# Optimization experiments

Hardware: AMD Instinct MI355X
Metric: run time of the kernel (lower is better)

The kernel has to match this reference:

```python
import jax, jax.numpy as jnp
import numpy as np

D = 768
NH = 8
HD = D // NH
DFF = 2048
EPS = 1e-5


def _layer_norm(x, g, b):
    mu = jnp.mean(x, axis=-1, keepdims=True)
    var = jnp.mean(jnp.square(x - mu), axis=-1, keepdims=True)
    return (x - mu) * jax.lax.rsqrt(var + EPS) * g + b


def setup_inputs() -> dict:
    key = jax.random.key(0)
    ks = jax.random.split(key, 16)
    B, L = 2, 2048
    s = 0.02
    return {
        "x": jax.random.normal(ks[0], (B, L, D), jnp.float32),
        "attn_bias": jax.random.normal(ks[1], (B, L, L), jnp.float32),
        "in_proj_w": jax.random.normal(ks[2], (3 * D, D), jnp.float32) * s,
        "in_proj_b": jnp.zeros((3 * D,), jnp.float32),
        "out_w": jax.random.normal(ks[3], (D, D), jnp.float32) * s,
        "out_b": jnp.zeros((D,), jnp.float32),
        "W1": jax.random.normal(ks[4], (DFF, D), jnp.float32) * s,
        "b1": jnp.zeros((DFF,), jnp.float32),
        "W2": jax.random.normal(ks[5], (D, DFF), jnp.float32) * s,
        "b2": jnp.zeros((D,), jnp.float32),
        "g1": jnp.ones((D,), jnp.float32),
        "be1": jnp.zeros((D,), jnp.float32),
        "g2": jnp.ones((D,), jnp.float32),
        "be2": jnp.zeros((D,), jnp.float32),
    }


def reference(x, attn_bias, in_proj_w, in_proj_b, out_w, out_b,
              W1, b1, W2, b2, g1, be1, g2, be2):
    B, L, _ = x.shape
    # fused qkv projection (torch nn.MultiheadAttention in_proj)
    qkv = x @ in_proj_w.T + in_proj_b          # [B, L, 3D]
    q, k, v = jnp.split(qkv, 3, axis=-1)
    q = q.reshape(B, L, NH, HD).transpose(0, 2, 1, 3)  # [B, nH, L, hd]
    k = k.reshape(B, L, NH, HD).transpose(0, 2, 1, 3)
    v = v.reshape(B, L, NH, HD).transpose(0, 2, 1, 3)
    scale = 1.0 / jnp.sqrt(jnp.asarray(HD, x.dtype))
    scores = jnp.einsum("bhqd,bhkd->bhqk", q * scale, k)
    scores = scores + attn_bias[:, None, :, :]         # broadcast over heads == expand
    attn = jax.nn.softmax(scores, axis=-1)
    ctx = jnp.einsum("bhqk,bhkd->bhqd", attn, v)       # [B, nH, L, hd]
    ctx = ctx.transpose(0, 2, 1, 3).reshape(B, L, D)
    attn_out = ctx @ out_w.T + out_b
    x = _layer_norm(x + attn_out, g1, be1)
    h = jax.nn.gelu(x @ W1.T + b1, approximate=False)  # torch default GELU = erf
    ff = h @ W2.T + b2
    return _layer_norm(x + ff, g2, be2)
```

## Files before the change

kernel.cpp:

```cpp
#include <hip/hip_runtime.h>
#include <hip/hip_bf16.h>
#include <math.h>

typedef __bf16 bf16;
typedef __attribute__((ext_vector_type(8))) __bf16 bf16x8;
typedef __attribute__((ext_vector_type(4))) __bf16 bf16x4;
typedef __attribute__((ext_vector_type(2))) __bf16 bf16x2;
typedef __attribute__((ext_vector_type(4))) float f32x4;
typedef __attribute__((ext_vector_type(2))) unsigned uint2v;

#define LOG2E 1.4426950408889634f

__device__ __forceinline__ void gload16(const bf16* g, bf16* l) {
  __builtin_amdgcn_global_load_lds(
      (const __attribute__((address_space(1))) void*)g,
      (__attribute__((address_space(3))) void*)l, 16, 0, 0);
}

__device__ __forceinline__ unsigned packbf2(float a, float b) {
  bf16x2 v = { (bf16)a, (bf16)b };
  return __builtin_bit_cast(unsigned, v);
}

__device__ __forceinline__ unsigned shx32u(unsigned v) {
#if __has_builtin(__builtin_amdgcn_permlane32_swap)
  uint2v r = __builtin_amdgcn_permlane32_swap(v, v, false, false);
  return (threadIdx.x & 32) ? r[0] : r[1];
#else
  return __shfl_xor(v, 32);
#endif
}
__device__ __forceinline__ unsigned shx16u(unsigned v) {
#if __has_builtin(__builtin_amdgcn_permlane16_swap)
  uint2v r = __builtin_amdgcn_permlane16_swap(v, v, false, false);
  return (threadIdx.x & 16) ? r[0] : r[1];
#else
  return __shfl_xor(v, 16);
#endif
}
__device__ __forceinline__ float shx32f(float v) {
  return __builtin_bit_cast(float, shx32u(__builtin_bit_cast(unsigned, v)));
}
__device__ __forceinline__ float shx16f(float v) {
  return __builtin_bit_cast(float, shx16u(__builtin_bit_cast(unsigned, v)));
}

__device__ __forceinline__ int xcd_swz(int id, int nwg) {
  return (id & 7) * (nwg >> 3) + (id >> 3);
}

struct CastSegs { const float* src[5]; bf16* dst[5]; };

__global__ void fused_cast_kernel(CastSegs segs) {
  const int e0 = 786432, e1 = 1228800, e2 = 1376256, e3 = 1769472, e4 = 2162688;
  int i = blockIdx.x * blockDim.x + threadIdx.x;
  int stride = gridDim.x * blockDim.x;
  for (; i < e4; i += stride) {
    int s = 0, base = 0;
    if (i >= e0) { s = 1; base = e0; }
    if (i >= e1) { s = 2; base = e1; }
    if (i >= e2) { s = 3; base = e2; }
    if (i >= e3) { s = 4; base = e3; }
    float4 v = ((const float4*)segs.src[s])[i - base];
    bf16x4 o = { (bf16)v.x, (bf16)v.y, (bf16)v.z, (bf16)v.w };
    ((bf16x4*)segs.dst[s])[i - base] = o;
  }
}

template<int MODE>
__launch_bounds__(256)
__global__ void gemm_kernel(const bf16* __restrict__ A, const bf16* __restrict__ W,
                            const float* __restrict__ bias, bf16* __restrict__ vt,
                            void* __restrict__ out, int K, int O) {
  __shared__ bf16 As[128 * 64];
  __shared__ bf16 Bs[128 * 64];
  const int gx = gridDim.x;
  const int id = blockIdx.y * gx + blockIdx.x;
  const int swz = xcd_swz(id, gx * gridDim.y);
  const int n0 = (swz / gx) * 128;
  const int o0 = (swz % gx) * 128;
  const int t    = threadIdx.x;
  const int lane = t & 63;
  const int wave = t >> 6;
  const int wr = (wave >> 1) * 64;
  const int wc = (wave & 1) * 64;

  f32x4 zero = {0.f, 0.f, 0.f, 0.f};
  f32x4 acc[4][4];
#pragma unroll
  for (int m = 0; m < 4; m++)
#pragma unroll
    for (int n = 0; n < 4; n++) acc[m][n] = zero;

  const int fr  = lane & 15;
  const int fg8 = (lane >> 4) * 8;

  for (int k0 = 0; k0 < K; k0 += 64) {
    __syncthreads();
#pragma unroll
    for (int c = 0; c < 4; c++) {
      int f = c * 256 + t;
      int row = f >> 3;
      int col = (f & 7) * 8;
      gload16(&A[(size_t)(n0 + row) * K + k0 + col], &As[f * 8]);
      gload16(&W[(size_t)(o0 + row) * K + k0 + col], &Bs[f * 8]);
    }
    __syncthreads();
#pragma unroll
    for (int kf = 0; kf < 2; kf++) {
      bf16x8 a[4], b[4];
#pragma unroll
      for (int m = 0; m < 4; m++) a[m] = *(const bf16x8*)&As[(wr + m * 16 + fr) * 64 + kf * 32 + fg8];
#pragma unroll
      for (int n = 0; n < 4; n++) b[n] = *(const bf16x8*)&Bs[(wc + n * 16 + fr) * 64 + kf * 32 + fg8];
#pragma unroll
      for (int m = 0; m < 4; m++)
#pragma unroll
        for (int n = 0; n < 4; n++)
          acc[m][n] = __builtin_amdgcn_mfma_f32_16x16x32_bf16(a[m], b[n], acc[m][n], 0, 0, 0);
    }
  }

  const int fg4 = (lane >> 4) * 4;
#pragma unroll
  for (int m = 0; m < 4; m++) {
#pragma unroll
    for (int n = 0; n < 4; n++) {
      int col = o0 + wc + n * 16 + fr;
      float bv = bias[col];
      if constexpr (MODE == 3) {
        if (col >= 1536) {
          int c = col - 1536;
          int h = c / 96;
          int hd = c - h * 96;
          int row0 = n0 + wr + m * 16 + fg4;
          int b = row0 >> 11;
          int token = row0 & 2047;
          bf16x4 ov;
#pragma unroll
          for (int r = 0; r < 4; r++) ov[r] = (bf16)(acc[m][n][r] + bv);
          *(bf16x4*)&vt[((size_t)((b * 8 + h) * 96 + hd)) * 2048 + token] = ov;
          continue;
        }
      }
#pragma unroll
      for (int r = 0; r < 4; r++) {
        int row = n0 + wr + m * 16 + fg4 + r;
        float v = acc[m][n][r] + bv;
        if constexpr (MODE == 2) {
          v = 0.5f * v * (1.0f + erff(v * 0.70710678118654752f));
          ((bf16*)out)[(size_t)row * O + col] = (bf16)v;
        } else {
          ((bf16*)out)[(size_t)row * O + col] = (bf16)v;
        }
      }
    }
  }
}

__launch_bounds__(256)
__global__ void gemmSK_kernel(const bf16* __restrict__ A, const bf16* __restrict__ W,
                              float* __restrict__ out, int K, int O) {
  __shared__ bf16 As[128 * 64];
  __shared__ bf16 Bs[128 * 64];
  const int gx = gridDim.x;
  const int id = blockIdx.y * gx + blockIdx.x;
  const int swz = xcd_swz(id, gx * gridDim.y);
  const int n0 = (swz / gx) * 128;
  const int o0 = (swz % gx) * 128;
  const int t    = threadIdx.x;
  const int lane = t & 63;
  const int wave = t >> 6;
  const int wr = (wave >> 1) * 64;
  const int wc = (wave & 1) * 64;
  const int khalf = K >> 1;
  const int kbeg = blockIdx.z * khalf;

  f32x4 zero = {0.f, 0.f, 0.f, 0.f};
  f32x4 acc[4][4];
#pragma unroll
  for (int m = 0; m < 4; m++)
#pragma unroll
    for (int n = 0; n < 4; n++) acc[m][n] = zero;

  const int fr  = lane & 15;
  const int fg8 = (lane >> 4) * 8;

  for (int k0 = kbeg; k0 < kbeg + khalf; k0 += 64) {
    __syncthreads();
#pragma unroll
    for (int c = 0; c < 4; c++) {
      int f = c * 256 + t;
      int row = f >> 3;
      int col = (f & 7) * 8;
      gload16(&A[(size_t)(n0 + row) * K + k0 + col], &As[f * 8]);
      gload16(&W[(size_t)(o0 + row) * K + k0 + col], &Bs[f * 8]);
    }
    __syncthreads();
#pragma unroll
    for (int kf = 0; kf < 2; kf++) {
      bf16x8 a[4], b[4];
#pragma unroll
      for (int m = 0; m < 4; m++) a[m] = *(const bf16x8*)&As[(wr + m * 16 + fr) * 64 + kf * 32 + fg8];
#pragma unroll
      for (int n = 0; n < 4; n++) b[n] = *(const bf16x8*)&Bs[(wc + n * 16 + fr) * 64 + kf * 32 + fg8];
#pragma unroll
      for (int m = 0; m < 4; m++)
#pragma unroll
        for (int n = 0; n < 4; n++)
          acc[m][n] = __builtin_amdgcn_mfma_f32_16x16x32_bf16(a[m], b[n], acc[m][n], 0, 0, 0);
    }
  }

  float* op = out + (size_t)blockIdx.z * 4096 * O;
  const int fg4 = (lane >> 4) * 4;
#pragma unroll
  for (int m = 0; m < 4; m++) {
#pragma unroll
    for (int n = 0; n < 4; n++) {
      int col = o0 + wc + n * 16 + fr;
#pragma unroll
      for (int r = 0; r < 4; r++) {
        int row = n0 + wr + m * 16 + fg4 + r;
        op[(size_t)row * O + col] = acc[m][n][r];
      }
    }
  }
}

__launch_bounds__(256, 4)
__global__ void attn_kernel(const bf16* __restrict__ qkv, const bf16* __restrict__ vt,
                            const float* __restrict__ bias, bf16* __restrict__ ctx) {
  __shared__ bf16 Ks[64 * 96];
  __shared__ bf16 Vs[96 * 64];
  const int t    = threadIdx.x;
  const int lane = t & 63;
  const int wave = t >> 6;
  const int bid = blockIdx.x;
  const int xcd = bid & 7, j = bid >> 3;
  const int h = j & 7;
  const int g_ = xcd * 8 + (j >> 3);
  const int qb = g_ & 31;
  const int b  = g_ >> 5;
  const int q0 = qb * 64 + wave * 16;
  const int fq = lane & 15;
  const int g  = lane >> 4;
  const size_t base = (size_t)b * 2048 * 2304;

  bf16x8 qf[3];
  {
    const bf16* qp = qkv + base + (size_t)(q0 + fq) * 2304 + h * 96;
#pragma unroll
    for (int f = 0; f < 3; f++) qf[f] = *(const bf16x8*)(qp + f * 32 + g * 8);
  }

  const int krow = t >> 2, kg = t & 3;
  const int ksw = kg ^ (krow & 3);
  const int vrow0 = t >> 3, vc = t & 7;
  const int vsw = vc ^ (vrow0 & 7);
  const bf16* kbase = qkv + base + 768 + h * 96;
  const bf16* vbase = vt + (size_t)((b * 8 + h) * 96) * 2048;

  bf16x8 kreg[3], vreg[3];
#pragma unroll
  for (int i = 0; i < 3; i++) {
    kreg[i] = *(const bf16x8*)(kbase + (size_t)krow * 2304 + i * 32 + kg * 8);
    vreg[i] = *(const bf16x8*)(vbase + (size_t)(vrow0 + 32 * i) * 2048 + vc * 8);
  }

  float l_run = 0.f;
  f32x4 zero = {0.f, 0.f, 0.f, 0.f};
  f32x4 o_acc[6];
#pragma unroll
  for (int i = 0; i < 6; i++) o_acc[i] = zero;

  const float scl2 = 0.10206207261596575f * LOG2E;
  const float* bp = bias + ((size_t)b * 2048 + q0 + fq) * 2048;

  float4 bfv[4];
#pragma unroll
  for (int kvt = 0; kvt < 4; kvt++) {
    float4 bv = *(const float4*)(bp + kvt * 16 + g * 4);
    bfv[kvt] = make_float4(bv.x * LOG2E, bv.y * LOG2E, bv.z * LOG2E, bv.w * LOG2E);
  }

  const int krd = fq * 96 + (g ^ (fq & 3)) * 8;
  const int vrd0 = fq * 64 + ((0 * 4 + g) ^ (fq & 7)) * 8;
  const int vrd1 = fq * 64 + ((1 * 4 + g) ^ (fq & 7)) * 8;

  for (int kv0 = 0; kv0 < 2048; kv0 += 64) {
    if (kv0) __syncthreads();
#pragma unroll
    for (int i = 0; i < 3; i++) {
      *(bf16x8*)&Ks[(krow * 12 + i * 4 + ksw) * 8] = kreg[i];
      *(bf16x8*)&Vs[((vrow0 + 32 * i) * 8 + vsw) * 8] = vreg[i];
    }
    if (kv0 + 64 < 2048) {
      int nx = kv0 + 64;
#pragma unroll
      for (int i = 0; i < 3; i++) {
        kreg[i] = *(const bf16x8*)(kbase + (size_t)(nx + krow) * 2304 + i * 32 + kg * 8);
        vreg[i] = *(const bf16x8*)(vbase + (size_t)(vrow0 + 32 * i) * 2048 + nx + vc * 8);
      }
    }
    __builtin_amdgcn_sched_barrier(0);
    __syncthreads();

    f32x4 s[4];
    __builtin_amdgcn_s_setprio(1);
#pragma unroll
    for (int kvt = 0; kvt < 4; kvt++) {
      s[kvt] = zero;
#pragma unroll
      for (int f = 0; f < 3; f++) {
        bf16x8 kfr = *(const bf16x8*)&Ks[kvt * 1536 + krd + f * 32];
        s[kvt] = __builtin_amdgcn_mfma_f32_16x16x32_bf16(kfr, qf[f], s[kvt], 0, 0, 0);
      }
    }
    __builtin_amdgcn_s_setprio(0);

    float rsum = 0.f;
    uint2 d[4];
#pragma unroll
    for (int kvt = 0; kvt < 4; kvt++) {
      float e0 = exp2f(fmaf(s[kvt][0], scl2, (&bfv[kvt].x)[0]));
      float e1 = exp2f(fmaf(s[kvt][1], scl2, (&bfv[kvt].x)[1]));
      float e2 = exp2f(fmaf(s[kvt][2], scl2, (&bfv[kvt].x)[2]));
      float e3 = exp2f(fmaf(s[kvt][3], scl2, (&bfv[kvt].x)[3]));
      rsum += (e0 + e1) + (e2 + e3);
      d[kvt].x = packbf2(e0, e1);
      d[kvt].y = packbf2(e2, e3);
    }
    l_run += rsum;

    {
      int nxb = (kv0 + 64) & 2047;
#pragma unroll
      for (int kvt = 0; kvt < 4; kvt++) {
        float4 bv = *(const float4*)(bp + nxb + kvt * 16 + g * 4);
        bfv[kvt] = make_float4(bv.x * LOG2E, bv.y * LOG2E, bv.z * LOG2E, bv.w * LOG2E);
      }
    }

    bf16x8 pb[2];
    {
      bool glow = (g < 2);
      uint2 snd0 = glow ? d[1] : d[0];
      uint2 snd1 = glow ? d[3] : d[2];
      uint2 r0, r1;
      r0.x = shx32u(snd0.x); r0.y = shx32u(snd0.y);
      r1.x = shx32u(snd1.x); r1.y = shx32u(snd1.y);
      uint2 k0 = glow ? d[0] : d[1];
      uint2 k1 = glow ? d[2] : d[3];
      bool sendk = ((g ^ (g >> 1)) & 1);
      uint2 s0 = sendk ? k0 : r0;
      uint2 s1 = sendk ? k1 : r1;
      uint2 q0_, q1_;
      q0_.x = shx16u(s0.x); q0_.y = shx16u(s0.y);
      q1_.x = shx16u(s1.x); q1_.y = shx16u(s1.y);
      uint2 kept0 = sendk ? r0 : k0;
      uint2 kept1 = sendk ? r1 : k1;
      bool godd = (g & 1);
      uint2 lo0 = godd ? q0_ : kept0;
      uint2 hi0 = godd ? kept0 : q0_;
      uint2 lo1 = godd ? q1_ : kept1;
      uint2 hi1 = godd ? kept1 : q1_;
      uint4 u0 = { lo0.x, lo0.y, hi0.x, hi0.y };
      uint4 u1 = { lo1.x, lo1.y, hi1.x, hi1.y };
      pb[0] = __builtin_bit_cast(bf16x8, u0);
      pb[1] = __builtin_bit_cast(bf16x8, u1);
    }

    __builtin_amdgcn_s_setprio(1);
#pragma unroll
    for (int ht = 0; ht < 6; ht++) {
      bf16x8 v0 = *(const bf16x8*)&Vs[ht * 1024 + vrd0];
      o_acc[ht] = __builtin_amdgcn_mfma_f32_16x16x32_bf16(v0, pb[0], o_acc[ht], 0, 0, 0);
      bf16x8 v1 = *(const bf16x8*)&Vs[ht * 1024 + vrd1];
      o_acc[ht] = __builtin_amdgcn_mfma_f32_16x16x32_bf16(v1, pb[1], o_acc[ht], 0, 0, 0);
    }
    __builtin_amdgcn_s_setprio(0);
  }

  l_run += shx16f(l_run);
  l_run += shx32f(l_run);
  float inv = 1.0f / l_run;
  bf16* cp = ctx + ((size_t)b * 2048 + q0 + fq) * 768 + h * 96;
#pragma unroll
  for (int ht = 0; ht < 6; ht++) {
    bf16x4 ov;
#pragma unroll
    for (int r = 0; r < 4; r++) ov[r] = (bf16)(o_acc[ht][r] * inv);
    *(bf16x4*)(cp + ht * 16 + g * 4) = ov;
  }
}

__launch_bounds__(256)
__global__ void lnf_kernel(const float* __restrict__ p0, const float* __restrict__ p1,
                           const float* __restrict__ bias, const float* __restrict__ res,
                           const float* __restrict__ gamma, const float* __restrict__ beta,
                           float* __restrict__ outf, bf16* __restrict__ outb) {
  const int row = blockIdx.x;
  const int t = threadIdx.x;
  const size_t off = (size_t)row * 768;
  float v[3];
#pragma unroll
  for (int i = 0; i < 3; i++) {
    int col = t + 256 * i;
    v[i] = p0[off + col] + p1[off + col] + bias[col] + res[off + col];
  }
  float s = v[0] + v[1] + v[2];
  float ss = v[0] * v[0] + v[1] * v[1] + v[2] * v[2];
#pragma unroll
  for (int o = 1; o < 64; o <<= 1) {
    s += __shfl_xor(s, o);
    ss += __shfl_xor(ss, o);
  }
  __shared__ float red[8];
  if ((t & 63) == 0) { red[(t >> 6) * 2] = s; red[(t >> 6) * 2 + 1] = ss; }
  __syncthreads();
  s = red[0] + red[2] + red[4] + red[6];
  ss = red[1] + red[3] + red[5] + red[7];
  float mu = s * (1.0f / 768.0f);
  float var = ss * (1.0f / 768.0f) - mu * mu;
  float rs = rsqrtf(var + 1e-5f);
#pragma unroll
  for (int i = 0; i < 3; i++) {
    int col = t + 256 * i;
    float y = (v[i] - mu) * rs * gamma[col] + beta[col];
    outf[off + col] = y;
    if (outb) outb[off + col] = (bf16)y;
  }
}

extern "C" void kernel_launch(void* const* d_in, const int* in_sizes, int n_in,
                              void* d_out, int out_size, void* d_ws, size_t ws_size,
                              hipStream_t stream) {
  (void)in_sizes; (void)n_in; (void)out_size; (void)ws_size;
  const float* x     = (const float*)d_in[0];
  const float* ab    = (const float*)d_in[1];
  const float* w_qkv = (const float*)d_in[2];
  const float* b_qkv = (const float*)d_in[3];
  const float* w_out = (const float*)d_in[4];
  const float* b_out = (const float*)d_in[5];
  const float* W1    = (const float*)d_in[6];
  const float* b1    = (const float*)d_in[7];
  const float* W2    = (const float*)d_in[8];
  const float* b2    = (const float*)d_in[9];
  const float* g1    = (const float*)d_in[10];
  const float* be1   = (const float*)d_in[11];
  const float* g2    = (const float*)d_in[12];
  const float* be2   = (const float*)d_in[13];
  float* outf = (float*)d_out;

  char* p = (char*)d_ws;
  bf16* xb    = (bf16*)p;  p += (size_t)4096 * 768 * 2;
  bf16* qkv   = (bf16*)p;  p += (size_t)4096 * 2304 * 2;
  bf16* ctx   = (bf16*)p;  p += (size_t)4096 * 768 * 2;
  float* x1f  = (float*)p; p += (size_t)4096 * 768 * 4;
  bf16* x1b   = (bf16*)p;  p += (size_t)4096 * 768 * 2;
  bf16* hbuf  = (bf16*)p;  p += (size_t)4096 * 2048 * 2;
  bf16* wqkvb = (bf16*)p;  p += (size_t)2304 * 768 * 2;
  bf16* woutb = (bf16*)p;  p += (size_t)768 * 768 * 2;
  bf16* w1b   = (bf16*)p;  p += (size_t)2048 * 768 * 2;
  bf16* w2b   = (bf16*)p;  p += (size_t)768 * 2048 * 2;
  float* pSK  = (float*)p; p += (size_t)2 * 4096 * 768 * 4;
  bf16* vtb   = (bf16*)x1f;

  CastSegs segs;
  segs.src[0] = x;     segs.dst[0] = xb;
  segs.src[1] = w_qkv; segs.dst[1] = wqkvb;
  segs.src[2] = w_out; segs.dst[2] = woutb;
  segs.src[3] = W1;    segs.dst[3] = w1b;
  segs.src[4] = W2;    segs.dst[4] = w2b;
  fused_cast_kernel<<<2048, 256, 0, stream>>>(segs);

  gemm_kernel<3><<<dim3(18, 32), 256, 0, stream>>>(xb, wqkvb, b_qkv, vtb, qkv, 768, 2304);
  attn_kernel<<<512, 256, 0, stream>>>(qkv, vtb, ab, ctx);
  gemmSK_kernel<<<dim3(6, 32, 2), 256, 0, stream>>>(ctx, woutb, pSK, 768, 768);
  lnf_kernel<<<4096, 256, 0, stream>>>(pSK, pSK + (size_t)4096 * 768, b_out, x, g1, be1, x1f, x1b);
  gemm_kernel<2><<<dim3(16, 32), 256, 0, stream>>>(x1b, w1b, b1, nullptr, hbuf, 768, 2048);
  gemmSK_kernel<<<dim3(6, 32, 2), 256, 0, stream>>>(hbuf, w2b, pSK, 2048, 768);
  lnf_kernel<<<4096, 256, 0, stream>>>(pSK, pSK + (size_t)4096 * 768, b2, x1f, g2, be2, outf, nullptr);
}
```

Baseline: 208.5 us.

## Split KV range across two wave groups per attention block and merge via LDS

The attention kernel now launches 512 threads per block. Two groups of four waves each process half of the 2048 keys for the same 64 queries, each group using its own double-sized K/V LDS buffer. After the loop, group 0 writes its partial output accumulators and row sums into LDS and group 1 adds them before normalising and storing. This doubles the waves available to hide latency over the long sequential KV loop. The cost is an extra LDS exchange and sync at the end, plus higher LDS and register pressure per block, which may limit occupancy.

```diff
diff --git a/kernel.cpp b/kernel.cpp
--- a/kernel.cpp
+++ b/kernel.cpp
@@ -228,21 +228,25 @@
   }
 }
 
-__launch_bounds__(256, 4)
+__launch_bounds__(512, 2)
 __global__ void attn_kernel(const bf16* __restrict__ qkv, const bf16* __restrict__ vt,
                             const float* __restrict__ bias, bf16* __restrict__ ctx) {
-  __shared__ bf16 Ks[64 * 96];
-  __shared__ bf16 Vs[96 * 64];
+  __shared__ bf16 Ks[2][64 * 96];
+  __shared__ bf16 Vs[2][96 * 64];
   const int t    = threadIdx.x;
   const int lane = t & 63;
   const int wave = t >> 6;
+  const int grp  = wave >> 2;
+  const int wv   = wave & 3;
+  const int tg   = t & 255;
   const int bid = blockIdx.x;
   const int xcd = bid & 7, j = bid >> 3;
   const int h = j & 7;
   const int g_ = xcd * 8 + (j >> 3);
   const int qb = g_ & 31;
   const int b  = g_ >> 5;
-  const int q0 = qb * 64 + wave * 16;
+  const int kvstart = grp * 1024;
+  const int q0 = qb * 64 + wv * 16;
   const int fq = lane & 15;
   const int g  = lane >> 4;
   const size_t base = (size_t)b * 2048 * 2304;
@@ -254,12 +258,12 @@
     for (int f = 0; f < 3; f++) qf[f] = *(const bf16x8*)(qp + f * 32 + g * 8);
   }
 
-  const int krow = t >> 2, kg = t & 3;
+  const int krow = tg >> 2, kg = tg & 3;
   const int ksw = kg ^ (krow & 3);
-  const int vrow0 = t >> 3, vc = t & 7;
+  const int vrow0 = tg >> 3, vc = tg & 7;
   const int vsw = vc ^ (vrow0 & 7);
-  const bf16* kbase = qkv + base + 768 + h * 96;
-  const bf16* vbase = vt + (size_t)((b * 8 + h) * 96) * 2048;
+  const bf16* kbase = qkv + base + (size_t)kvstart * 2304 + 768 + h * 96;
+  const bf16* vbase = vt + (size_t)((b * 8 + h) * 96) * 2048 + kvstart;
 
   bf16x8 kreg[3], vreg[3];
 #pragma unroll
@@ -275,7 +279,7 @@
   for (int i = 0; i < 6; i++) o_acc[i] = zero;
 
   const float scl2 = 0.10206207261596575f * LOG2E;
-  const float* bp = bias + ((size_t)b * 2048 + q0 + fq) * 2048;
+  const float* bp = bias + ((size_t)b * 2048 + q0 + fq) * 2048 + kvstart;
 
   float4 bfv[4];
 #pragma unroll
@@ -288,14 +292,14 @@
   const int vrd0 = fq * 64 + ((0 * 4 + g) ^ (fq & 7)) * 8;
   const int vrd1 = fq * 64 + ((1 * 4 + g) ^ (fq & 7)) * 8;
 
-  for (int kv0 = 0; kv0 < 2048; kv0 += 64) {
+  for (int kv0 = 0; kv0 < 1024; kv0 += 64) {
     if (kv0) __syncthreads();
 #pragma unroll
     for (int i = 0; i < 3; i++) {
-      *(bf16x8*)&Ks[(krow * 12 + i * 4 + ksw) * 8] = kreg[i];
-      *(bf16x8*)&Vs[((vrow0 + 32 * i) * 8 + vsw) * 8] = vreg[i];
-    }
-    if (kv0 + 64 < 2048) {
+      *(bf16x8*)&Ks[grp][(krow * 12 + i * 4 + ksw) * 8] = kreg[i];
+      *(bf16x8*)&Vs[grp][((vrow0 + 32 * i) * 8 + vsw) * 8] = vreg[i];
+    }
+    if (kv0 + 64 < 1024) {
       int nx = kv0 + 64;
 #pragma unroll
       for (int i = 0; i < 3; i++) {
@@ -313,7 +317,7 @@
       s[kvt] = zero;
 #pragma unroll
       for (int f = 0; f < 3; f++) {
-        bf16x8 kfr = *(const bf16x8*)&Ks[kvt * 1536 + krd + f * 32];
+        bf16x8 kfr = *(const bf16x8*)&Ks[grp][kvt * 1536 + krd + f * 32];
         s[kvt] = __builtin_amdgcn_mfma_f32_16x16x32_bf16(kfr, qf[f], s[kvt], 0, 0, 0);
       }
     }
@@ -334,7 +338,7 @@
     l_run += rsum;
 
     {
-      int nxb = (kv0 + 64) & 2047;
+      int nxb = (kv0 + 64) & 1023;
 #pragma unroll
       for (int kvt = 0; kvt < 4; kvt++) {
         float4 bv = *(const float4*)(bp + nxb + kvt * 16 + g * 4);
@@ -374,9 +378,9 @@
     __builtin_amdgcn_s_setprio(1);
 #pragma unroll
     for (int ht = 0; ht < 6; ht++) {
-      bf16x8 v0 = *(const bf16x8*)&Vs[ht * 1024 + vrd0];
+      bf16x8 v0 = *(const bf16x8*)&Vs[grp][ht * 1024 + vrd0];
       o_acc[ht] = __builtin_amdgcn_mfma_f32_16x16x32_bf16(v0, pb[0], o_acc[ht], 0, 0, 0);
-      bf16x8 v1 = *(const bf16x8*)&Vs[ht * 1024 + vrd1];
+      bf16x8 v1 = *(const bf16x8*)&Vs[grp][ht * 1024 + vrd1];
       o_acc[ht] = __builtin_amdgcn_mfma_f32_16x16x32_bf16(v1, pb[1], o_acc[ht], 0, 0, 0);
     }
     __builtin_amdgcn_s_setprio(0);
@@ -384,14 +388,30 @@
 
   l_run += shx16f(l_run);
   l_run += shx32f(l_run);
-  float inv = 1.0f / l_run;
-  bf16* cp = ctx + ((size_t)b * 2048 + q0 + fq) * 768 + h * 96;
-#pragma unroll
-  for (int ht = 0; ht < 6; ht++) {
-    bf16x4 ov;
-#pragma unroll
-    for (int r = 0; r < 4; r++) ov[r] = (bf16)(o_acc[ht][r] * inv);
-    *(bf16x4*)(cp + ht * 16 + g * 4) = ov;
+
+  float* exch = (float*)&Ks[0][0];
+  float* lex  = (float*)&Vs[0][0];
+  const int qi = wv * 16 + fq;
+
+  __syncthreads();
+  if (grp == 0) {
+#pragma unroll
+    for (int ht = 0; ht < 6; ht++)
+      *(f32x4*)&exch[qi * 96 + ht * 16 + g * 4] = o_acc[ht];
+    if (g == 0) lex[qi] = l_run;
+  }
+  __syncthreads();
+  if (grp == 1) {
+    float inv = 1.0f / (l_run + lex[qi]);
+    bf16* cp = ctx + ((size_t)b * 2048 + q0 + fq) * 768 + h * 96;
+#pragma unroll
+    for (int ht = 0; ht < 6; ht++) {
+      f32x4 o1 = *(const f32x4*)&exch[qi * 96 + ht * 16 + g * 4];
+      bf16x4 ov;
+#pragma unroll
+      for (int r = 0; r < 4; r++) ov[r] = (bf16)((o_acc[ht][r] + o1[r]) * inv);
+      *(bf16x4*)(cp + ht * 16 + g * 4) = ov;
+    }
   }
 }
 
@@ -476,7 +496,7 @@
   fused_cast_kernel<<<2048, 256, 0, stream>>>(segs);
 
   gemm_kernel<3><<<dim3(18, 32), 256, 0, stream>>>(xb, wqkvb, b_qkv, vtb, qkv, 768, 2304);
-  attn_kernel<<<512, 256, 0, stream>>>(qkv, vtb, ab, ctx);
+  attn_kernel<<<512, 512, 0, stream>>>(qkv, vtb, ab, ctx);
   gemmSK_kernel<<<dim3(6, 32, 2), 256, 0, stream>>>(ctx, woutb, pSK, 768, 768);
   lnf_kernel<<<4096, 256, 0, stream>>>(pSK, pSK + (size_t)4096 * 768, b_out, x, g1, be1, x1f, x1b);
   gemm_kernel<2><<<dim3(16, 32), 256, 0, stream>>>(x1b, w1b, b1, nullptr, hbuf, 768, 2048);
```

After: 223.7 us. 1.07x slower.
